# Performance work log

Hardware: AMD Instinct MI355X
Metric: run time of the kernel (lower is better)

Reference implementation:

```python
import jax, jax.numpy as jnp
import numpy as np
from jax import lax

POOL = 4  # hp['gcn_pool_size']


def sparsemax(z):
    # sparsemax along last axis (Martins & Astudillo 2016), matches tfa.activations.sparsemax
    n = z.shape[-1]
    z_sorted = jnp.flip(jnp.sort(z, axis=-1), axis=-1)          # descending
    k = jnp.arange(1, n + 1, dtype=z.dtype)
    zcum = jnp.cumsum(z_sorted, axis=-1)
    support = (1.0 + k * z_sorted) > zcum                        # [.., n] bool
    k_sel = jnp.sum(support, axis=-1, keepdims=True)             # int, >= 1
    tau = (jnp.take_along_axis(zcum, k_sel - 1, axis=-1) - 1.0) / k_sel.astype(z.dtype)
    return jnp.maximum(z - tau, 0.0)


def gcn_layer(x, W):
    # x: [B, T, E]
    T = x.shape[1]
    # einsum('Bte,bte->tBb') then mean over t == contract over t,e and divide by T
    adj = jnp.einsum('Bte,bte->Bb', x, x) / T                    # [B, B]
    adj = sparsemax(adj)                                         # row-wise sparsemax
    m = adj[:, :, None, None] * x[None]                          # [B, b, T, E] outer product
    # MaxPool2D((POOL,1), stride 1, 'same') on [batch=B, H=b, W=T, C=E]: pool over neighbor axis b
    m = lax.reduce_window(m, -jnp.inf, lax.max,
                          (1, POOL, 1, 1), (1, 1, 1, 1), 'SAME')
    agg = jnp.sum(m, axis=1)                                     # [B, T, E]
    return jax.nn.relu(agg @ W)                                  # [B, T, rel_dim]


def setup_inputs() -> dict:
    key = jax.random.key(0)
    k0, k1, k2, k3 = jax.random.split(key, 4)
    B, T, E = 64, 256, 64
    rel_dim, n_stack = 4, 8
    x = jax.random.normal(k0, (B, T, E), dtype=jnp.float32)
    W0 = jax.random.normal(k1, (E, rel_dim), dtype=jnp.float32) * 0.1
    W1 = jax.random.normal(k2, (rel_dim, rel_dim), dtype=jnp.float32) * 0.1
    Wp = jax.random.normal(k3, (rel_dim, n_stack), dtype=jnp.float32) * 0.1
    return {"x": x, "W0": W0, "W1": W1, "Wp": Wp}


def reference(x, W0, W1, Wp):
    x = gcn_layer(x, W0)           # layer 0: E -> rel_dim
    x = gcn_layer(x, W1)           # layer 1: rel_dim -> rel_dim
    pooled = jnp.mean(x, axis=1)   # [B, rel_dim], mean over T
    return jax.nn.softmax(pooled @ Wp, axis=-1)  # [B, n_stack]
```

## Files before the change

kernel.cpp:

```cpp
#include <hip/hip_runtime.h>
#include <math.h>

__device__ __forceinline__ float4 f4max(float4 a, float4 b) {
    return make_float4(fmaxf(a.x, b.x), fmaxf(a.y, b.y), fmaxf(a.z, b.z), fmaxf(a.w, b.w));
}
__device__ __forceinline__ float4 f4scale(float s, float4 v) {
    return make_float4(s * v.x, s * v.y, s * v.z, s * v.w);
}
__device__ __forceinline__ float4 f4add(float4 a, float4 b) {
    return make_float4(a.x + b.x, a.y + b.y, a.z + b.z, a.w + b.w);
}
__device__ __forceinline__ float4 f4fma(float a, float4 b, float4 c) {
    return make_float4(fmaf(a, b.x, c.x), fmaf(a, b.y, c.y), fmaf(a, b.z, c.z), fmaf(a, b.w, c.w));
}
__device__ __forceinline__ float4 f4fma4(float4 a, float4 b, float4 c) {
    return make_float4(fmaf(a.x, b.x, c.x), fmaf(a.y, b.y, c.y),
                       fmaf(a.z, b.z, c.z), fmaf(a.w, b.w, c.w));
}

__device__ __forceinline__ float wave_sparsemax(float z, int lane) {
    float v = z;
    for (int k = 2; k <= 64; k <<= 1) {
        bool desc = (lane & k) == 0;
        for (int j = k >> 1; j > 0; j >>= 1) {
            float other = __shfl_xor(v, j, 64);
            bool lower = (lane & j) == 0;
            float mn = fminf(v, other), mx = fmaxf(v, other);
            v = (desc ^ lower) ? mn : mx;
        }
    }
    float c = v;
    for (int d = 1; d < 64; d <<= 1) {
        float n = __shfl_up(c, d, 64);
        if (lane >= d) c += n;
    }
    bool sup = (1.0f + (float)(lane + 1) * v) > c;
    int ksel = __popcll(__ballot(sup));
    float zk = __shfl(c, ksel - 1, 64);
    float tau = (zk - 1.0f) / (float)ksel;
    return fmaxf(z - tau, 0.f);
}

__global__ __launch_bounds__(256)
void gram_partial(const float* __restrict__ X, float* __restrict__ P) {
    __shared__ float xsT[64][68];
    int tid = threadIdx.x;
    int k0 = blockIdx.x * 64;
#pragma unroll
    for (int it = 0; it < 4; ++it) {
        int f = it * 256 + tid;
        int i = f >> 4, k4 = (f & 15) * 4;
        float4 v = *(const float4*)(X + (size_t)i * 16384 + k0 + k4);
        xsT[k4 + 0][i] = v.x; xsT[k4 + 1][i] = v.y;
        xsT[k4 + 2][i] = v.z; xsT[k4 + 3][i] = v.w;
    }
    __syncthreads();
    int ti = (tid >> 4) * 4, tj = (tid & 15) * 4;
    float4 a0 = make_float4(0, 0, 0, 0), a1 = a0, a2 = a0, a3 = a0;
#pragma unroll 8
    for (int k = 0; k < 64; ++k) {
        float4 a = *(const float4*)&xsT[k][ti];
        float4 b = *(const float4*)&xsT[k][tj];
        a0 = f4fma(a.x, b, a0); a1 = f4fma(a.y, b, a1);
        a2 = f4fma(a.z, b, a2); a3 = f4fma(a.w, b, a3);
    }
    float* basep = P + ((size_t)blockIdx.x << 12);
    *(float4*)(basep + (ti + 0) * 64 + tj) = a0;
    *(float4*)(basep + (ti + 1) * 64 + tj) = a1;
    *(float4*)(basep + (ti + 2) * 64 + tj) = a2;
    *(float4*)(basep + (ti + 3) * 64 + tj) = a3;
}

__global__ __launch_bounds__(256)
void reduce_sm(const float* __restrict__ P, float* __restrict__ adj0) {
    __shared__ float red[4 * 64];
    int tid = threadIdx.x;
    int row = blockIdx.x;
    int w = tid >> 6;
    int lane = tid & 63;
    float s = 0.f;
    for (int c = w * 64; c < (w + 1) * 64; ++c)
        s += P[((size_t)c << 12) + row * 64 + lane];
    red[w * 64 + lane] = s;
    __syncthreads();
    if (tid < 64) {
        float z = (red[lane] + red[64 + lane] + red[128 + lane] + red[192 + lane])
                  * (1.0f / 256.0f);
        adj0[row * 64 + lane] = wave_sparsemax(z, lane);
    }
}

__global__ __launch_bounds__(256)
void agg0_kernel(const float* __restrict__ x, const float* __restrict__ adj0,
                 const float* __restrict__ W0, float* __restrict__ h0) {
    int tid = threadIdx.x;
    int lane = tid & 63;
    int w = __builtin_amdgcn_readfirstlane(tid >> 6);
    int t0 = (blockIdx.x >> 3) * 4;
    int Bc = (blockIdx.x & 7) * 8;
    int t = lane >> 4, eq = lane & 15;
    const float* pA = adj0 + (Bc + 2 * w) * 64;
    const float* pB = pA + 64;
    float4 w0r0 = *(const float4*)(W0 + (eq * 4 + 0) * 4);
    float4 w0r1 = *(const float4*)(W0 + (eq * 4 + 1) * 4);
    float4 w0r2 = *(const float4*)(W0 + (eq * 4 + 2) * 4);
    float4 w0r3 = *(const float4*)(W0 + (eq * 4 + 3) * 4);
    const float4* xg = (const float4*)(x + ((size_t)(t0 + t) * 64) + eq * 4);
    float4 x4 = xg[0];
    float4 vA = f4scale(pA[0], x4), vB = f4scale(pB[0], x4);
    float4 qm1A = vA, qm1B = vB;
    x4 = xg[4096];
    float4 vtA = f4scale(pA[1], x4), vtB = f4scale(pB[1], x4);
    float4 qbA = f4max(vA, vtA), qbB = f4max(vB, vtB);
    float4 accA = make_float4(0, 0, 0, 0), accB = accA;
#pragma unroll 8
    for (int bl = 0; bl < 62; ++bl) {
        x4 = xg[(size_t)(bl + 2) * 4096];
        float4 vnA = f4scale(pA[bl + 2], x4);
        float4 vnB = f4scale(pB[bl + 2], x4);
        float4 q1A = f4max(vtA, vnA), q1B = f4max(vtB, vnB);
        accA = f4add(accA, f4max(qm1A, q1A));
        accB = f4add(accB, f4max(qm1B, q1B));
        qm1A = qbA; qbA = q1A; vtA = vnA;
        qm1B = qbB; qbB = q1B; vtB = vnB;
    }
    accA = f4add(accA, f4max(qm1A, vtA));
    accB = f4add(accB, f4max(qm1B, vtB));
    accA = f4add(accA, qbA);
    accB = f4add(accB, qbB);
#pragma unroll
    for (int half = 0; half < 2; ++half) {
        float4 acc = half ? accB : accA;
        float4 h = f4fma(acc.x, w0r0, f4fma(acc.y, w0r1,
                   f4fma(acc.z, w0r2, f4scale(acc.w, w0r3))));
        for (int m = 1; m <= 8; m <<= 1) {
            h.x += __shfl_xor(h.x, m, 64);
            h.y += __shfl_xor(h.y, m, 64);
            h.z += __shfl_xor(h.z, m, 64);
            h.w += __shfl_xor(h.w, m, 64);
        }
        if (eq == 0) {
            int B = Bc + 2 * w + half;
            float4 r = make_float4(fmaxf(h.x, 0.f), fmaxf(h.y, 0.f),
                                   fmaxf(h.z, 0.f), fmaxf(h.w, 0.f));
            *(float4*)(h0 + (size_t)(B * 256 + t0 + t) * 4) = r;
        }
    }
}

__global__ __launch_bounds__(256)
void tail_kernel(const float* __restrict__ h0, const float* __restrict__ W1,
                 const float* __restrict__ Wp, float* __restrict__ out) {
    __shared__ __align__(16) float row[4 * 260];
    __shared__ float part[256];
    __shared__ float psm[64];
    __shared__ float red[16];
    int tid = threadIdx.x;
    int lane = tid & 63;
    int bid = blockIdx.x;
    {
        int q = tid >> 6, s = (tid & 63) * 4;
        *(float4*)(row + q * 260 + s) = *(const float4*)(h0 + (size_t)bid * 1024 + tid * 4);
    }
    __syncthreads();
    {
        int j = tid >> 2, q = tid & 3;
        const float4* hj = (const float4*)(h0 + (size_t)j * 1024 + q * 256);
        const float4* ri = (const float4*)(row + q * 260);
        float4 s4 = make_float4(0, 0, 0, 0);
#pragma unroll 8
        for (int kk = 0; kk < 64; ++kk) s4 = f4fma4(ri[kk], hj[kk], s4);
        part[tid] = s4.x + s4.y + s4.z + s4.w;
    }
    __syncthreads();
    if (tid < 64) {
        float z = (part[lane * 4] + part[lane * 4 + 1] + part[lane * 4 + 2]
                   + part[lane * 4 + 3]) * (1.0f / 256.0f);
        psm[lane] = wave_sparsemax(z, lane);
    }
    __syncthreads();
    int w = __builtin_amdgcn_readfirstlane(tid >> 6);
    int rc = lane & 3;
    float psum = 0.f;
#pragma unroll
    for (int gg = 0; gg < 4; ++gg) {
        int tbase = w * 64 + gg * 16;
        const float* xb = h0 + (size_t)tbase * 4 + lane;
        float v0 = psm[0] * xb[0];
        float v1 = psm[1] * xb[1024];
        float qm1 = v0, qb = fmaxf(v0, v1), vt = v1, acc = 0.f;
#pragma unroll 8
        for (int bl = 0; bl < 62; ++bl) {
            float vn = psm[bl + 2] * xb[(size_t)(bl + 2) * 1024];
            float q1 = fmaxf(vt, vn);
            acc += fmaxf(qm1, q1);
            qm1 = qb; qb = q1; vt = vn;
        }
        acc += fmaxf(qm1, vt);
        acc += qb;
        int base = lane & ~3;
        float b0 = __shfl(acc, base + 0, 64);
        float b1 = __shfl(acc, base + 1, 64);
        float b2 = __shfl(acc, base + 2, 64);
        float b3 = __shfl(acc, base + 3, 64);
        float h = b0 * W1[rc] + b1 * W1[4 + rc] + b2 * W1[8 + rc] + b3 * W1[12 + rc];
        psum += fmaxf(h, 0.f);
    }
    for (int m = 4; m <= 32; m <<= 1) psum += __shfl_xor(psum, m, 64);
    if (lane < 4) red[w * 4 + lane] = psum;
    __syncthreads();
    if (tid < 64) {
        float pooled = 0.f;
        if (lane < 4)
            pooled = (red[lane] + red[4 + lane] + red[8 + lane] + red[12 + lane])
                     * (1.0f / 256.0f);
        float q0 = __shfl(pooled, 0, 64), q1 = __shfl(pooled, 1, 64);
        float q2 = __shfl(pooled, 2, 64), q3 = __shfl(pooled, 3, 64);
        float logit = -INFINITY;
        if (lane < 8)
            logit = q0 * Wp[lane] + q1 * Wp[8 + lane]
                  + q2 * Wp[16 + lane] + q3 * Wp[24 + lane];
        float mx = logit;
        for (int m = 4; m >= 1; m >>= 1) mx = fmaxf(mx, __shfl_xor(mx, m, 8));
        float e = (lane < 8) ? __expf(logit - mx) : 0.f;
        float s = e;
        for (int m = 4; m >= 1; m >>= 1) s += __shfl_xor(s, m, 8);
        if (lane < 8) out[bid * 8 + lane] = e / s;
    }
}

extern "C" void kernel_launch(void* const* d_in, const int* in_sizes, int n_in,
                              void* d_out, int out_size, void* d_ws, size_t ws_size,
                              hipStream_t stream) {
    const float* x  = (const float*)d_in[0];
    const float* W0 = (const float*)d_in[1];
    const float* W1 = (const float*)d_in[2];
    const float* Wp = (const float*)d_in[3];
    float* out = (float*)d_out;

    char* ws = (char*)d_ws;
    float* P    = (float*)ws;
    float* adj0 = (float*)(ws + (4u << 20));
    float* h0   = (float*)(ws + (4u << 20) + 16384);

    gram_partial<<<256, 256, 0, stream>>>(x, P);
    reduce_sm<<<64, 256, 0, stream>>>(P, adj0);
    agg0_kernel<<<512, 256, 0, stream>>>(x, adj0, W0, h0);
    tail_kernel<<<64, 256, 0, stream>>>(h0, W1, Wp, out);
}
```

Measured before the change: 118.9 us.

## Fuse four GCN kernels into one cooperative kernel with grid syncs

Merges the gram partial, reduce+sparsemax, layer-0 aggregation and tail kernels into one cooperative launch of 256 blocks separated by grid-wide barriers. The layer-0 aggregation is remapped so each block handles 16 batch rows instead of 8, which fits the 256-block grid and reuses each x load across four adjacency rows. The aim is to remove the overhead of three extra kernel launches. In exchange the reduce and tail phases use only 64 of the 256 blocks while the rest idle at barriers, and grid.sync adds its own cost.

```diff
diff --git a/kernel.cpp b/kernel.cpp
--- a/kernel.cpp
+++ b/kernel.cpp
@@ -1,5 +1,8 @@
 #include <hip/hip_runtime.h>
+#include <hip/hip_cooperative_groups.h>
 #include <math.h>
+
+namespace cg = cooperative_groups;
 
 __device__ __forceinline__ float4 f4max(float4 a, float4 b) {
     return make_float4(fmaxf(a.x, b.x), fmaxf(a.y, b.y), fmaxf(a.z, b.z), fmaxf(a.w, b.w));
@@ -42,190 +45,193 @@
 }
 
 __global__ __launch_bounds__(256)
-void gram_partial(const float* __restrict__ X, float* __restrict__ P) {
+void fused_gcn(const float* __restrict__ x, const float* __restrict__ W0,
+               const float* __restrict__ W1, const float* __restrict__ Wp,
+               float* __restrict__ P, float* __restrict__ adj0,
+               float* __restrict__ h0, float* __restrict__ out) {
+    cg::grid_group grid = cg::this_grid();
     __shared__ float xsT[64][68];
-    int tid = threadIdx.x;
-    int k0 = blockIdx.x * 64;
-#pragma unroll
-    for (int it = 0; it < 4; ++it) {
-        int f = it * 256 + tid;
-        int i = f >> 4, k4 = (f & 15) * 4;
-        float4 v = *(const float4*)(X + (size_t)i * 16384 + k0 + k4);
-        xsT[k4 + 0][i] = v.x; xsT[k4 + 1][i] = v.y;
-        xsT[k4 + 2][i] = v.z; xsT[k4 + 3][i] = v.w;
-    }
-    __syncthreads();
-    int ti = (tid >> 4) * 4, tj = (tid & 15) * 4;
-    float4 a0 = make_float4(0, 0, 0, 0), a1 = a0, a2 = a0, a3 = a0;
-#pragma unroll 8
-    for (int k = 0; k < 64; ++k) {
-        float4 a = *(const float4*)&xsT[k][ti];
-        float4 b = *(const float4*)&xsT[k][tj];
-        a0 = f4fma(a.x, b, a0); a1 = f4fma(a.y, b, a1);
-        a2 = f4fma(a.z, b, a2); a3 = f4fma(a.w, b, a3);
-    }
-    float* basep = P + ((size_t)blockIdx.x << 12);
-    *(float4*)(basep + (ti + 0) * 64 + tj) = a0;
-    *(float4*)(basep + (ti + 1) * 64 + tj) = a1;
-    *(float4*)(basep + (ti + 2) * 64 + tj) = a2;
-    *(float4*)(basep + (ti + 3) * 64 + tj) = a3;
-}
-
-__global__ __launch_bounds__(256)
-void reduce_sm(const float* __restrict__ P, float* __restrict__ adj0) {
-    __shared__ float red[4 * 64];
-    int tid = threadIdx.x;
-    int row = blockIdx.x;
-    int w = tid >> 6;
-    int lane = tid & 63;
-    float s = 0.f;
-    for (int c = w * 64; c < (w + 1) * 64; ++c)
-        s += P[((size_t)c << 12) + row * 64 + lane];
-    red[w * 64 + lane] = s;
-    __syncthreads();
-    if (tid < 64) {
-        float z = (red[lane] + red[64 + lane] + red[128 + lane] + red[192 + lane])
-                  * (1.0f / 256.0f);
-        adj0[row * 64 + lane] = wave_sparsemax(z, lane);
-    }
-}
-
-__global__ __launch_bounds__(256)
-void agg0_kernel(const float* __restrict__ x, const float* __restrict__ adj0,
-                 const float* __restrict__ W0, float* __restrict__ h0) {
-    int tid = threadIdx.x;
-    int lane = tid & 63;
-    int w = __builtin_amdgcn_readfirstlane(tid >> 6);
-    int t0 = (blockIdx.x >> 3) * 4;
-    int Bc = (blockIdx.x & 7) * 8;
-    int t = lane >> 4, eq = lane & 15;
-    const float* pA = adj0 + (Bc + 2 * w) * 64;
-    const float* pB = pA + 64;
-    float4 w0r0 = *(const float4*)(W0 + (eq * 4 + 0) * 4);
-    float4 w0r1 = *(const float4*)(W0 + (eq * 4 + 1) * 4);
-    float4 w0r2 = *(const float4*)(W0 + (eq * 4 + 2) * 4);
-    float4 w0r3 = *(const float4*)(W0 + (eq * 4 + 3) * 4);
-    const float4* xg = (const float4*)(x + ((size_t)(t0 + t) * 64) + eq * 4);
-    float4 x4 = xg[0];
-    float4 vA = f4scale(pA[0], x4), vB = f4scale(pB[0], x4);
-    float4 qm1A = vA, qm1B = vB;
-    x4 = xg[4096];
-    float4 vtA = f4scale(pA[1], x4), vtB = f4scale(pB[1], x4);
-    float4 qbA = f4max(vA, vtA), qbB = f4max(vB, vtB);
-    float4 accA = make_float4(0, 0, 0, 0), accB = accA;
-#pragma unroll 8
-    for (int bl = 0; bl < 62; ++bl) {
-        x4 = xg[(size_t)(bl + 2) * 4096];
-        float4 vnA = f4scale(pA[bl + 2], x4);
-        float4 vnB = f4scale(pB[bl + 2], x4);
-        float4 q1A = f4max(vtA, vnA), q1B = f4max(vtB, vnB);
-        accA = f4add(accA, f4max(qm1A, q1A));
-        accB = f4add(accB, f4max(qm1B, q1B));
-        qm1A = qbA; qbA = q1A; vtA = vnA;
-        qm1B = qbB; qbB = q1B; vtB = vnB;
-    }
-    accA = f4add(accA, f4max(qm1A, vtA));
-    accB = f4add(accB, f4max(qm1B, vtB));
-    accA = f4add(accA, qbA);
-    accB = f4add(accB, qbB);
-#pragma unroll
-    for (int half = 0; half < 2; ++half) {
-        float4 acc = half ? accB : accA;
-        float4 h = f4fma(acc.x, w0r0, f4fma(acc.y, w0r1,
-                   f4fma(acc.z, w0r2, f4scale(acc.w, w0r3))));
-        for (int m = 1; m <= 8; m <<= 1) {
-            h.x += __shfl_xor(h.x, m, 64);
-            h.y += __shfl_xor(h.y, m, 64);
-            h.z += __shfl_xor(h.z, m, 64);
-            h.w += __shfl_xor(h.w, m, 64);
-        }
-        if (eq == 0) {
-            int B = Bc + 2 * w + half;
-            float4 r = make_float4(fmaxf(h.x, 0.f), fmaxf(h.y, 0.f),
-                                   fmaxf(h.z, 0.f), fmaxf(h.w, 0.f));
-            *(float4*)(h0 + (size_t)(B * 256 + t0 + t) * 4) = r;
-        }
-    }
-}
-
-__global__ __launch_bounds__(256)
-void tail_kernel(const float* __restrict__ h0, const float* __restrict__ W1,
-                 const float* __restrict__ Wp, float* __restrict__ out) {
+    __shared__ float redB[256];
     __shared__ __align__(16) float row[4 * 260];
     __shared__ float part[256];
     __shared__ float psm[64];
     __shared__ float red[16];
+
     int tid = threadIdx.x;
+    int bx = blockIdx.x;
     int lane = tid & 63;
-    int bid = blockIdx.x;
+
     {
-        int q = tid >> 6, s = (tid & 63) * 4;
-        *(float4*)(row + q * 260 + s) = *(const float4*)(h0 + (size_t)bid * 1024 + tid * 4);
-    }
-    __syncthreads();
+        int k0 = bx * 64;
+#pragma unroll
+        for (int it = 0; it < 4; ++it) {
+            int f = it * 256 + tid;
+            int i = f >> 4, k4 = (f & 15) * 4;
+            float4 v = *(const float4*)(x + (size_t)i * 16384 + k0 + k4);
+            xsT[k4 + 0][i] = v.x; xsT[k4 + 1][i] = v.y;
+            xsT[k4 + 2][i] = v.z; xsT[k4 + 3][i] = v.w;
+        }
+        __syncthreads();
+        int ti = (tid >> 4) * 4, tj = (tid & 15) * 4;
+        float4 a0 = make_float4(0, 0, 0, 0), a1 = a0, a2 = a0, a3 = a0;
+#pragma unroll 8
+        for (int k = 0; k < 64; ++k) {
+            float4 a = *(const float4*)&xsT[k][ti];
+            float4 b = *(const float4*)&xsT[k][tj];
+            a0 = f4fma(a.x, b, a0); a1 = f4fma(a.y, b, a1);
+            a2 = f4fma(a.z, b, a2); a3 = f4fma(a.w, b, a3);
+        }
+        float* basep = P + ((size_t)bx << 12);
+        *(float4*)(basep + (ti + 0) * 64 + tj) = a0;
+        *(float4*)(basep + (ti + 1) * 64 + tj) = a1;
+        *(float4*)(basep + (ti + 2) * 64 + tj) = a2;
+        *(float4*)(basep + (ti + 3) * 64 + tj) = a3;
+    }
+    grid.sync();
+
+    if (bx < 64) {
+        int w = tid >> 6;
+        float s = 0.f;
+        for (int c = w * 64; c < (w + 1) * 64; ++c)
+            s += P[((size_t)c << 12) + bx * 64 + lane];
+        redB[w * 64 + lane] = s;
+        __syncthreads();
+        if (tid < 64) {
+            float z = (redB[lane] + redB[64 + lane] + redB[128 + lane] + redB[192 + lane])
+                      * (1.0f / 256.0f);
+            adj0[bx * 64 + lane] = wave_sparsemax(z, lane);
+        }
+    }
+    grid.sync();
+
     {
-        int j = tid >> 2, q = tid & 3;
-        const float4* hj = (const float4*)(h0 + (size_t)j * 1024 + q * 256);
-        const float4* ri = (const float4*)(row + q * 260);
-        float4 s4 = make_float4(0, 0, 0, 0);
+        int t0 = (bx >> 2) * 4;
+        int Bc = (bx & 3) * 16;
+        int w = __builtin_amdgcn_readfirstlane(tid >> 6);
+        int t = lane >> 4, eq = lane & 15;
+        const float* pr0 = adj0 + (size_t)(Bc + 4 * w) * 64;
+        float4 w0r0 = *(const float4*)(W0 + (eq * 4 + 0) * 4);
+        float4 w0r1 = *(const float4*)(W0 + (eq * 4 + 1) * 4);
+        float4 w0r2 = *(const float4*)(W0 + (eq * 4 + 2) * 4);
+        float4 w0r3 = *(const float4*)(W0 + (eq * 4 + 3) * 4);
+        const float4* xg = (const float4*)(x + ((size_t)(t0 + t) * 64) + eq * 4);
+        float4 qm1[4], qb[4], vt[4], acc[4];
+        float4 xA = xg[0];
+        float4 xB = xg[4096];
+#pragma unroll
+        for (int h = 0; h < 4; ++h) {
+            const float* p = pr0 + h * 64;
+            float4 v = f4scale(p[0], xA);
+            vt[h] = f4scale(p[1], xB);
+            qm1[h] = v;
+            qb[h] = f4max(v, vt[h]);
+            acc[h] = make_float4(0, 0, 0, 0);
+        }
+#pragma unroll 4
+        for (int bl = 0; bl < 62; ++bl) {
+            float4 xn = xg[(size_t)(bl + 2) * 4096];
+#pragma unroll
+            for (int h = 0; h < 4; ++h) {
+                float4 vn = f4scale(pr0[h * 64 + bl + 2], xn);
+                float4 q1 = f4max(vt[h], vn);
+                acc[h] = f4add(acc[h], f4max(qm1[h], q1));
+                qm1[h] = qb[h]; qb[h] = q1; vt[h] = vn;
+            }
+        }
+#pragma unroll
+        for (int h = 0; h < 4; ++h) {
+            acc[h] = f4add(acc[h], f4max(qm1[h], vt[h]));
+            acc[h] = f4add(acc[h], qb[h]);
+            float4 a = acc[h];
+            float4 hh = f4fma(a.x, w0r0, f4fma(a.y, w0r1,
+                       f4fma(a.z, w0r2, f4scale(a.w, w0r3))));
+            for (int m = 1; m <= 8; m <<= 1) {
+                hh.x += __shfl_xor(hh.x, m, 64);
+                hh.y += __shfl_xor(hh.y, m, 64);
+                hh.z += __shfl_xor(hh.z, m, 64);
+                hh.w += __shfl_xor(hh.w, m, 64);
+            }
+            if (eq == 0) {
+                int B = Bc + 4 * w + h;
+                float4 r = make_float4(fmaxf(hh.x, 0.f), fmaxf(hh.y, 0.f),
+                                       fmaxf(hh.z, 0.f), fmaxf(hh.w, 0.f));
+                *(float4*)(h0 + (size_t)(B * 256 + t0 + t) * 4) = r;
+            }
+        }
+    }
+    grid.sync();
+
+    if (bx < 64) {
+        int bid = bx;
+        {
+            int q = tid >> 6, s2 = (tid & 63) * 4;
+            *(float4*)(row + q * 260 + s2) = *(const float4*)(h0 + (size_t)bid * 1024 + tid * 4);
+        }
+        __syncthreads();
+        {
+            int j = tid >> 2, q = tid & 3;
+            const float4* hj = (const float4*)(h0 + (size_t)j * 1024 + q * 256);
+            const float4* ri = (const float4*)(row + q * 260);
+            float4 s4 = make_float4(0, 0, 0, 0);
 #pragma unroll 8
-        for (int kk = 0; kk < 64; ++kk) s4 = f4fma4(ri[kk], hj[kk], s4);
-        part[tid] = s4.x + s4.y + s4.z + s4.w;
-    }
-    __syncthreads();
-    if (tid < 64) {
-        float z = (part[lane * 4] + part[lane * 4 + 1] + part[lane * 4 + 2]
-                   + part[lane * 4 + 3]) * (1.0f / 256.0f);
-        psm[lane] = wave_sparsemax(z, lane);
-    }
-    __syncthreads();
-    int w = __builtin_amdgcn_readfirstlane(tid >> 6);
-    int rc = lane & 3;
-    float psum = 0.f;
-#pragma unroll
-    for (int gg = 0; gg < 4; ++gg) {
-        int tbase = w * 64 + gg * 16;
-        const float* xb = h0 + (size_t)tbase * 4 + lane;
-        float v0 = psm[0] * xb[0];
-        float v1 = psm[1] * xb[1024];
-        float qm1 = v0, qb = fmaxf(v0, v1), vt = v1, acc = 0.f;
+            for (int kk = 0; kk < 64; ++kk) s4 = f4fma4(ri[kk], hj[kk], s4);
+            part[tid] = s4.x + s4.y + s4.z + s4.w;
+        }
+        __syncthreads();
+        if (tid < 64) {
+            float z = (part[lane * 4] + part[lane * 4 + 1] + part[lane * 4 + 2]
+                       + part[lane * 4 + 3]) * (1.0f / 256.0f);
+            psm[lane] = wave_sparsemax(z, lane);
+        }
+        __syncthreads();
+        int w = __builtin_amdgcn_readfirstlane(tid >> 6);
+        int rc = lane & 3;
+        float psum = 0.f;
+#pragma unroll
+        for (int gg = 0; gg < 4; ++gg) {
+            int tbase = w * 64 + gg * 16;
+            const float* xb = h0 + (size_t)tbase * 4 + lane;
+            float v0 = psm[0] * xb[0];
+            float v1 = psm[1] * xb[1024];
+            float qm1s = v0, qbs = fmaxf(v0, v1), vts = v1, accs = 0.f;
 #pragma unroll 8
-        for (int bl = 0; bl < 62; ++bl) {
-            float vn = psm[bl + 2] * xb[(size_t)(bl + 2) * 1024];
-            float q1 = fmaxf(vt, vn);
-            acc += fmaxf(qm1, q1);
-            qm1 = qb; qb = q1; vt = vn;
-        }
-        acc += fmaxf(qm1, vt);
-        acc += qb;
-        int base = lane & ~3;
-        float b0 = __shfl(acc, base + 0, 64);
-        float b1 = __shfl(acc, base + 1, 64);
-        float b2 = __shfl(acc, base + 2, 64);
-        float b3 = __shfl(acc, base + 3, 64);
-        float h = b0 * W1[rc] + b1 * W1[4 + rc] + b2 * W1[8 + rc] + b3 * W1[12 + rc];
-        psum += fmaxf(h, 0.f);
-    }
-    for (int m = 4; m <= 32; m <<= 1) psum += __shfl_xor(psum, m, 64);
-    if (lane < 4) red[w * 4 + lane] = psum;
-    __syncthreads();
-    if (tid < 64) {
-        float pooled = 0.f;
-        if (lane < 4)
-            pooled = (red[lane] + red[4 + lane] + red[8 + lane] + red[12 + lane])
-                     * (1.0f / 256.0f);
-        float q0 = __shfl(pooled, 0, 64), q1 = __shfl(pooled, 1, 64);
-        float q2 = __shfl(pooled, 2, 64), q3 = __shfl(pooled, 3, 64);
-        float logit = -INFINITY;
-        if (lane < 8)
-            logit = q0 * Wp[lane] + q1 * Wp[8 + lane]
-                  + q2 * Wp[16 + lane] + q3 * Wp[24 + lane];
-        float mx = logit;
-        for (int m = 4; m >= 1; m >>= 1) mx = fmaxf(mx, __shfl_xor(mx, m, 8));
-        float e = (lane < 8) ? __expf(logit - mx) : 0.f;
-        float s = e;
-        for (int m = 4; m >= 1; m >>= 1) s += __shfl_xor(s, m, 8);
-        if (lane < 8) out[bid * 8 + lane] = e / s;
+            for (int bl = 0; bl < 62; ++bl) {
+                float vn = psm[bl + 2] * xb[(size_t)(bl + 2) * 1024];
+                float q1 = fmaxf(vts, vn);
+                accs += fmaxf(qm1s, q1);
+                qm1s = qbs; qbs = q1; vts = vn;
+            }
+            accs += fmaxf(qm1s, vts);
+            accs += qbs;
+            int base = lane & ~3;
+            float b0 = __shfl(accs, base + 0, 64);
+            float b1 = __shfl(accs, base + 1, 64);
+            float b2 = __shfl(accs, base + 2, 64);
+            float b3 = __shfl(accs, base + 3, 64);
+            float h = b0 * W1[rc] + b1 * W1[4 + rc] + b2 * W1[8 + rc] + b3 * W1[12 + rc];
+            psum += fmaxf(h, 0.f);
+        }
+        for (int m = 4; m <= 32; m <<= 1) psum += __shfl_xor(psum, m, 64);
+        if (lane < 4) red[w * 4 + lane] = psum;
+        __syncthreads();
+        if (tid < 64) {
+            float pooled = 0.f;
+            if (lane < 4)
+                pooled = (red[lane] + red[4 + lane] + red[8 + lane] + red[12 + lane])
+                         * (1.0f / 256.0f);
+            float q0 = __shfl(pooled, 0, 64), q1 = __shfl(pooled, 1, 64);
+            float q2 = __shfl(pooled, 2, 64), q3 = __shfl(pooled, 3, 64);
+            float logit = -INFINITY;
+            if (lane < 8)
+                logit = q0 * Wp[lane] + q1 * Wp[8 + lane]
+                      + q2 * Wp[16 + lane] + q3 * Wp[24 + lane];
+            float mx = logit;
+            for (int m = 4; m >= 1; m >>= 1) mx = fmaxf(mx, __shfl_xor(mx, m, 8));
+            float e = (lane < 8) ? __expf(logit - mx) : 0.f;
+            float s = e;
+            for (int m = 4; m >= 1; m >>= 1) s += __shfl_xor(s, m, 8);
+            if (lane < 8) out[bid * 8 + lane] = e / s;
+        }
     }
 }
 
@@ -243,8 +249,8 @@
     float* adj0 = (float*)(ws + (4u << 20));
     float* h0   = (float*)(ws + (4u << 20) + 16384);
 
-    gram_partial<<<256, 256, 0, stream>>>(x, P);
-    reduce_sm<<<64, 256, 0, stream>>>(P, adj0);
-    agg0_kernel<<<512, 256, 0, stream>>>(x, adj0, W0, h0);
-    tail_kernel<<<64, 256, 0, stream>>>(h0, W1, Wp, out);
-}
+    void* args[8] = { (void*)&x, (void*)&W0, (void*)&W1, (void*)&Wp,
+                      (void*)&P, (void*)&adj0, (void*)&h0, (void*)&out };
+    hipLaunchCooperativeKernel(reinterpret_cast<void*>(fused_gcn),
+                               dim3(256), dim3(256), args, 0, stream);
+}
```

Result: slower. 211.2 us (+77.7%).
